# Performance work log

Hardware: AMD Instinct MI355X
Metric: run time of the kernel (lower is better)

## Reference

```python
import jax, jax.numpy as jnp
import numpy as np

GROUPS = 32
EPS = 1e-5


def group_norm(x, gamma, beta):
    # x: [b, h, w, c] NHWC; normalize over (h, w, c/GROUPS) within each group
    b, h, w, c = x.shape
    xg = x.reshape(b, h, w, GROUPS, c // GROUPS)
    mean = jnp.mean(xg, axis=(1, 2, 4), keepdims=True)
    var = jnp.var(xg, axis=(1, 2, 4), keepdims=True)
    xg = (xg - mean) * jax.lax.rsqrt(var + EPS)
    return xg.reshape(b, h, w, c) * gamma + beta


def setup_inputs() -> dict:
    key = jax.random.key(0)
    ks = jax.random.split(key, 6)
    c = 512
    s = 1.0 / np.sqrt(c)  # fan-in scaled init for conv weights
    return {
        "x": jax.random.normal(ks[0], (2, 64, 64, c), dtype=jnp.float32),
        "gamma": jnp.ones((c,), jnp.float32),
        "beta": jnp.zeros((c,), jnp.float32),
        "wq": jax.random.normal(ks[1], (c, c), jnp.float32) * s,
        "bq": jnp.zeros((c,), jnp.float32),
        "wk": jax.random.normal(ks[2], (c, c), jnp.float32) * s,
        "bk": jnp.zeros((c,), jnp.float32),
        "wv": jax.random.normal(ks[3], (c, c), jnp.float32) * s,
        "bv": jnp.zeros((c,), jnp.float32),
        "wo": jax.random.normal(ks[4], (c, c), jnp.float32) * s,
        "bo": jnp.zeros((c,), jnp.float32),
    }


def reference(x, gamma, beta, wq, bq, wk, bk, wv, bv, wo, bo):
    b, h, w, c = x.shape
    n = h * w
    hn = group_norm(x, gamma, beta)
    hn = hn.reshape(b, n, c)  # flatten spatial -> tokens
    # 1x1 convs == pointwise linear
    q = hn @ wq + bq  # [b, n, c]
    k = hn @ wk + bk
    v = hn @ wv + bv
    scores = jnp.einsum("bic,bjc->bij", q, k) * (c ** -0.5)  # [b, n, n]
    attn = jax.nn.softmax(scores, axis=-1)
    out = jnp.einsum("bij,bjc->bic", attn, v)  # [b, n, c]
    out = out @ wo + bo
    return x + out.reshape(b, h, w, c)
```

## Files before the change

### kernel.cpp

```cpp
#include <hip/hip_runtime.h>
#include <hip/hip_fp8.h>
#include <stdint.h>


typedef unsigned short u16;
typedef unsigned char u8;
typedef short s16x8 __attribute__((ext_vector_type(8)));
typedef float f32x4 __attribute__((ext_vector_type(4)));
typedef int i32x8 __attribute__((ext_vector_type(8)));
typedef float f32x16 __attribute__((ext_vector_type(16)));

#define NTOK 4096
#define CH   512

__device__ inline u16 f2bf(float f) {
  union { float f; uint32_t u; } v; v.f = f;
  uint32_t r = v.u + 0x7FFFu + ((v.u >> 16) & 1u);
  return (u16)(r >> 16);
}
__device__ inline float bf2f(u16 b) {
  union { uint32_t u; float f; } v; v.u = (uint32_t)b << 16; return v.f;
}
__device__ inline f32x4 mfma16(s16x8 a, s16x8 b, f32x4 c) {
  return __builtin_amdgcn_mfma_f32_16x16x32_bf16(a, b, c, 0, 0, 0);
}
__device__ inline f32x16 mfma_mx8(i32x8 a, i32x8 b, f32x16 c) {
  return __builtin_amdgcn_mfma_scale_f32_32x32x64_f8f6f4(
      a, b, c, 0 , 0 ,
      0, 0x7F7F7F7F, 0, 0x7F7F7F7F);
}
__device__ inline uint32_t pk_fp8x4(float e0, float e1, float e2, float e3) {
#if __has_builtin(__builtin_amdgcn_cvt_pk_fp8_f32)
  int v = __builtin_amdgcn_cvt_pk_fp8_f32(e0, e1, 0, false);
  v = __builtin_amdgcn_cvt_pk_fp8_f32(e2, e3, v, true);
  return (uint32_t)v;
#else
  __hip_fp8_e4m3 a(e0), b(e1), c(e2), d(e3);
  return (uint32_t)*(u8*)&a | ((uint32_t)*(u8*)&b << 8) |
         ((uint32_t)*(u8*)&c << 16) | ((uint32_t)*(u8*)&d << 24);
#endif
}
__device__ inline u8 f2fp8(float x) {
#if __has_builtin(__builtin_amdgcn_cvt_pk_fp8_f32)
  int v = __builtin_amdgcn_cvt_pk_fp8_f32(x, x, 0, false);
  return (u8)(v & 0xFF);
#else
  __hip_fp8_e4m3 h(x); return *(u8*)&h;
#endif
}
__device__ inline void gload_lds16(const void* g, void* l) {
  __builtin_amdgcn_global_load_lds(
      (const __attribute__((address_space(1))) unsigned*)g,
      (__attribute__((address_space(3))) unsigned*)l, 16, 0, 0);
}
__device__ inline uint4 addbf8(uint4 a, uint4 b) {
  union { uint4 v; u16 h[8]; } A, B, O; A.v = a; B.v = b;
#pragma unroll
  for (int j = 0; j < 8; j++) O.h[j] = f2bf(bf2f(A.h[j]) + bf2f(B.h[j]));
  return O.v;
}

__global__ __launch_bounds__(256) void gn_stats_kernel(
    const float* __restrict__ x, float* __restrict__ part) {
  int c = blockIdx.x, b = blockIdx.y;
  int t = threadIdx.x, g = t & 31;
  const float* xb = x + (size_t)b * NTOK * CH + (size_t)c * 64 * CH + g * 16;
  float s = 0.f, q = 0.f;
  for (int p = 0; p < 8; p++) {
    const float* ptr = xb + ((size_t)p * 8 + (t >> 5)) * CH;
#pragma unroll
    for (int j = 0; j < 4; j++) {
      float4 v = *(const float4*)(ptr + j * 4);
      s += v.x + v.y + v.z + v.w;
      q += v.x * v.x + v.y * v.y + v.z * v.z + v.w * v.w;
    }
  }
  __shared__ float ls[32][8], lq[32][8];
  ls[g][t >> 5] = s; lq[g][t >> 5] = q;
  __syncthreads();
  if (t < 32) {
    float S = 0.f, Q = 0.f;
#pragma unroll
    for (int j = 0; j < 8; j++) { S += ls[t][j]; Q += lq[t][j]; }
    float2 o; o.x = S; o.y = Q;
    *(float2*)&part[(((size_t)b * 64 + c) * 32 + t) * 2] = o;
  }
}

__global__ __launch_bounds__(256) void gn_apply_kernel(
    const float* __restrict__ x, const float* __restrict__ part,
    const float* __restrict__ gamma, const float* __restrict__ beta,
    u16* __restrict__ hn) {
  int blk = blockIdx.x, b = blk >> 9, t = threadIdx.x;
  __shared__ float msh[32], rsh[32];
  if (t < 64) {
    int g = t >> 1, half = t & 1;
    float S = 0.f, Q = 0.f;
    for (int c = half * 32; c < half * 32 + 32; c++) {
      float2 p = *(const float2*)&part[(((size_t)b * 64 + c) * 32 + g) * 2];
      S += p.x; Q += p.y;
    }
    S += __shfl_xor(S, 1, 64);
    Q += __shfl_xor(Q, 1, 64);
    if (half == 0) {
      float mean = S * (1.f / 65536.f);
      float var = Q * (1.f / 65536.f) - mean * mean;
      msh[g] = mean; rsh[g] = rsqrtf(var + 1e-5f);
    }
  }
  __syncthreads();
  size_t base = (size_t)b * NTOK * CH + (size_t)(blk & 511) * 4096 + t * 16;
  int ch0 = (t * 16) & 511;
  float mean = msh[t & 31], rstd = rsh[t & 31];
  const float* xp = x + base;
  union { u16 h[16]; uint4 v[2]; } o;
#pragma unroll
  for (int j = 0; j < 4; j++) {
    float4 xv = *(const float4*)(xp + j * 4);
    float4 gv = *(const float4*)(gamma + ch0 + j * 4);
    float4 bv = *(const float4*)(beta + ch0 + j * 4);
    o.h[j * 4 + 0] = f2bf((xv.x - mean) * rstd * gv.x + bv.x);
    o.h[j * 4 + 1] = f2bf((xv.y - mean) * rstd * gv.y + bv.y);
    o.h[j * 4 + 2] = f2bf((xv.z - mean) * rstd * gv.z + bv.z);
    o.h[j * 4 + 3] = f2bf((xv.w - mean) * rstd * gv.w + bv.w);
  }
  *(uint4*)(hn + base) = o.v[0];
  *(uint4*)(hn + base + 8) = o.v[1];
}

__global__ __launch_bounds__(256) void wprep_kernel(
    const float* w0, const float* w1, const float* w2, const float* w3,
    u16* t0, u16* t1, u16* t2, u16* t3) {
  int z = blockIdx.z;
  const float* w = z == 0 ? w0 : z == 1 ? w1 : z == 2 ? w2 : w3;
  u16* wt = z == 0 ? t0 : z == 1 ? t1 : z == 2 ? t2 : t3;
  __shared__ float tile[32][33];
  int k0 = blockIdx.x * 32, n0 = blockIdx.y * 32;
  int tx = threadIdx.x & 31, ty = threadIdx.x >> 5;
  for (int r = 0; r < 4; r++)
    tile[ty * 4 + r][tx] = w[(size_t)(k0 + ty * 4 + r) * CH + n0 + tx];
  __syncthreads();
  for (int r = 0; r < 4; r++)
    wt[(size_t)(n0 + ty * 4 + r) * CH + k0 + tx] = f2bf(tile[tx][ty * 4 + r]);
}

__global__ __launch_bounds__(256, 2) void qkv_gemm_kernel(
    const u16* __restrict__ A, const u16* __restrict__ Wcat,
    const float* __restrict__ bq, const float* __restrict__ bk,
    const float* __restrict__ bvv, u8* __restrict__ qf8, u8* __restrict__ kf8,
    u8* __restrict__ vtf8) {
  __shared__ __align__(16) u8 pool[65536];
  int m0 = blockIdx.x * 128, n0 = blockIdx.y * 128;
  int t = threadIdx.x, lane = t & 63, wave = t >> 6;
  int wx = wave & 1, wy = wave >> 1;
  int lane4 = lane >> 4;
  f32x4 acc[4][4] = {};
  const u16 *Asrc[4], *Bsrc[4];
  int dsto[4];
#pragma unroll
  for (int j = 0; j < 4; j++) {
    int u = t + j * 256, row = u >> 3, ch = (u & 7) ^ (row & 7);
    Asrc[j] = A + (size_t)(m0 + row) * CH + ch * 8;
    Bsrc[j] = Wcat + (size_t)(n0 + row) * CH + ch * 8;
    dsto[j] = u * 16;
  }
#pragma unroll
  for (int j = 0; j < 4; j++) {
    gload_lds16(Asrc[j], pool + dsto[j]);
    gload_lds16(Bsrc[j], pool + 32768 + dsto[j]);
  }
  __syncthreads();
  for (int kt = 0; kt < 8; kt++) {
    int co = (kt & 1) * 16384;
    const u16* Ac = (const u16*)(pool + co);
    const u16* Bc = (const u16*)(pool + 32768 + co);
    if (kt < 7) {
      int no = ((kt & 1) ^ 1) * 16384;
#pragma unroll
      for (int j = 0; j < 4; j++) {
        Asrc[j] += 64; Bsrc[j] += 64;
        gload_lds16(Asrc[j], pool + no + dsto[j]);
        gload_lds16(Bsrc[j], pool + 32768 + no + dsto[j]);
      }
    }
    __builtin_amdgcn_s_setprio(1);
#pragma unroll
    for (int ks = 0; ks < 2; ks++) {
      int kc = ks * 4 + lane4;
      s16x8 af[4], bf[4];
#pragma unroll
      for (int i = 0; i < 4; i++) {
        int ra = wx * 64 + i * 16 + (lane & 15);
        af[i] = *(const s16x8*)&Ac[ra * 64 + ((kc ^ (ra & 7)) << 3)];
        int rb = wy * 64 + i * 16 + (lane & 15);
        bf[i] = *(const s16x8*)&Bc[rb * 64 + ((kc ^ (rb & 7)) << 3)];
      }
#pragma unroll
      for (int mi = 0; mi < 4; mi++)
#pragma unroll
        for (int ni = 0; ni < 4; ni++)
          acc[mi][ni] = mfma16(af[mi], bf[ni], acc[mi][ni]);
    }
    __builtin_amdgcn_s_setprio(0);
    __syncthreads();
  }
  int proj = n0 >> 9;
  int r0l = wx * 64 + lane4 * 4;
  if (proj <= 1) {
    u8* O = proj == 0 ? qf8 : kf8;
    const float* bias = proj == 0 ? bq : bk;
#pragma unroll
    for (int mi = 0; mi < 4; mi++)
#pragma unroll
      for (int ni = 0; ni < 4; ni++) {
        int colp = (n0 & 511) + wy * 64 + ni * 16 + (lane & 15);
        float bv = bias[colp];
#pragma unroll
        for (int r = 0; r < 4; r++)
          O[(size_t)(m0 + r0l + mi * 16 + r) * CH + colp] =
              f2fp8(acc[mi][ni][r] + bv);
      }
  } else {
#pragma unroll
    for (int mi = 0; mi < 4; mi++)
#pragma unroll
      for (int ni = 0; ni < 4; ni++) {
        int colp = (n0 & 511) + wy * 64 + ni * 16 + (lane & 15);
        float bv = bvv[colp];
        int row = m0 + r0l + mi * 16;
        int bb = row >> 12, nn = row & 4095;
        uint32_t p = pk_fp8x4(acc[mi][ni][0] + bv, acc[mi][ni][1] + bv,
                              acc[mi][ni][2] + bv, acc[mi][ni][3] + bv);
        *(uint32_t*)&vtf8[((size_t)bb * CH + colp) * NTOK + nn] = p;
      }
  }
}

__global__ __launch_bounds__(256) void gemm_out_kernel(
    const u16* __restrict__ A, const u16* __restrict__ A2,
    const u16* __restrict__ Wt, const float* __restrict__ bias,
    float* __restrict__ out, const float* __restrict__ xres) {
  __shared__ __align__(16) u16 As[128 * 40];
  __shared__ __align__(16) u16 Bs[64 * 40];
  int m0 = blockIdx.x * 128, n0 = blockIdx.y * 64;
  int t = threadIdx.x, lane = t & 63, wave = t >> 6;
  int wm = wave >> 1, wn = wave & 1;
  f32x4 acc[4][2] = {};
  int arow = t >> 2, ac = t & 3;
  size_t aoff = (size_t)(m0 + arow) * CH + ac * 8;
  const u16* Bg = Wt + (size_t)(n0 + arow) * CH + ac * 8;
  uint4 a0 = addbf8(*(const uint4*)(A + aoff), *(const uint4*)(A2 + aoff));
  uint4 a1 = addbf8(*(const uint4*)(A + aoff + 64 * CH),
                    *(const uint4*)(A2 + aoff + 64 * CH));
  uint4 b0 = *(const uint4*)Bg;
  for (int kt = 0; kt < 16; kt++) {
    __syncthreads();
    *(uint4*)&As[(size_t)arow * 40 + ac * 8] = a0;
    *(uint4*)&As[(size_t)(arow + 64) * 40 + ac * 8] = a1;
    *(uint4*)&Bs[(size_t)arow * 40 + ac * 8] = b0;
    if (kt < 15) {
      aoff += 32; Bg += 32;
      a0 = addbf8(*(const uint4*)(A + aoff), *(const uint4*)(A2 + aoff));
      a1 = addbf8(*(const uint4*)(A + aoff + 64 * CH),
                  *(const uint4*)(A2 + aoff + 64 * CH));
      b0 = *(const uint4*)Bg;
    }
    __syncthreads();
    s16x8 af[4], bfr[2];
#pragma unroll
    for (int i = 0; i < 4; i++)
      af[i] = *(const s16x8*)&As[(wm * 64 + i * 16 + (lane & 15)) * 40 + (lane >> 4) * 8];
#pragma unroll
    for (int j = 0; j < 2; j++)
      bfr[j] = *(const s16x8*)&Bs[(wn * 32 + j * 16 + (lane & 15)) * 40 + (lane >> 4) * 8];
    __builtin_amdgcn_s_setprio(1);
#pragma unroll
    for (int mi = 0; mi < 4; mi++)
#pragma unroll
      for (int ni = 0; ni < 2; ni++)
        acc[mi][ni] = mfma16(af[mi], bfr[ni], acc[mi][ni]);
    __builtin_amdgcn_s_setprio(0);
  }
  int r0l = wm * 64 + ((lane >> 4) * 4);
  int c0l = wn * 32 + (lane & 15);
#pragma unroll
  for (int mi = 0; mi < 4; mi++)
#pragma unroll
    for (int ni = 0; ni < 2; ni++) {
      int col = n0 + c0l + ni * 16;
      float bv = bias[col];
#pragma unroll
      for (int r = 0; r < 4; r++) {
        size_t idx = (size_t)(m0 + r0l + mi * 16 + r) * CH + col;
        out[idx] = xres[idx] + acc[mi][ni][r] + bv;
      }
    }
}

__global__ __launch_bounds__(256, 2) void s_gemm_kernel(
    const u8* __restrict__ qf8, const u8* __restrict__ kf8,
    u8* __restrict__ S, float* __restrict__ lpart) {
  const float QS = 0.044194173824159216f;
  __shared__ __align__(16) u8 pool[65536];
  int bz = blockIdx.z;
  const u8* qb = qf8 + (size_t)bz * NTOK * CH;
  const u8* kb = kf8 + (size_t)bz * NTOK * CH;
  u8* Sg = S + (size_t)bz * NTOK * NTOK;
  float* lp = lpart + (size_t)bz * 64 * NTOK;
  int m0 = blockIdx.x * 128, n0 = blockIdx.y * 128;
  int t = threadIdx.x, lane = t & 63, wave = t >> 6;
  int wmx = wave & 1, wy = wave >> 1;
  int lh = lane >> 5;
  f32x16 acc[2][2] = {};
  const u8 *Asrc[4], *Bsrc[4];
  int dsto[4];
#pragma unroll
  for (int j = 0; j < 4; j++) {
    int u = t + j * 256, row = u >> 3, ch = (u & 7) ^ (row & 7);
    Asrc[j] = kb + (size_t)(n0 + row) * CH + ch * 16;
    Bsrc[j] = qb + (size_t)(m0 + row) * CH + ch * 16;
    dsto[j] = u * 16;
  }
#pragma unroll
  for (int j = 0; j < 4; j++) {
    gload_lds16(Asrc[j], pool + dsto[j]);
    gload_lds16(Bsrc[j], pool + 32768 + dsto[j]);
  }
  __syncthreads();
  for (int kt = 0; kt < 4; kt++) {
    int co = (kt & 1) * 16384;
    const u8* Ac = pool + co;
    const u8* Bc = pool + 32768 + co;
    if (kt < 3) {
      int no = ((kt & 1) ^ 1) * 16384;
#pragma unroll
      for (int j = 0; j < 4; j++) {
        Asrc[j] += 128; Bsrc[j] += 128;
        gload_lds16(Asrc[j], pool + no + dsto[j]);
        gload_lds16(Bsrc[j], pool + 32768 + no + dsto[j]);
      }
    }
    __builtin_amdgcn_s_setprio(1);
#pragma unroll
    for (int kh = 0; kh < 2; kh++) {
      int cb = kh * 4 + lh * 2;
      union { i32x8 v; uint4 qq[2]; } bu[2];
#pragma unroll
      for (int bj = 0; bj < 2; bj++) {
        int rb = wmx * 64 + bj * 32 + (lane & 31);
        const u8* bp = &Bc[rb * 128];
        bu[bj].qq[0] = *(const uint4*)&bp[(cb ^ (rb & 7)) << 4];
        bu[bj].qq[1] = *(const uint4*)&bp[((cb + 1) ^ (rb & 7)) << 4];
      }
#pragma unroll
      for (int ai = 0; ai < 2; ai++) {
        int ra = wy * 64 + ai * 32 + (lane & 31);
        union { i32x8 v; uint4 qq[2]; } au;
        const u8* ap = &Ac[ra * 128];
        au.qq[0] = *(const uint4*)&ap[(cb ^ (ra & 7)) << 4];
        au.qq[1] = *(const uint4*)&ap[((cb + 1) ^ (ra & 7)) << 4];
#pragma unroll
        for (int bj = 0; bj < 2; bj++)
          acc[ai][bj] = mfma_mx8(au.v, bu[bj].v, acc[ai][bj]);
      }
    }
    __builtin_amdgcn_s_setprio(0);
    __syncthreads();
  }
  uint32_t* Stile = (uint32_t*)pool;
  float psum[2] = {};
#pragma unroll
  for (int ai = 0; ai < 2; ai++) {
#pragma unroll
    for (int bj = 0; bj < 2; bj++) {
      int ml = wmx * 64 + bj * 32 + (lane & 31);
#pragma unroll
      for (int qd = 0; qd < 4; qd++) {
        float e0 = __expf(acc[ai][bj][qd * 4 + 0] * QS);
        float e1 = __expf(acc[ai][bj][qd * 4 + 1] * QS);
        float e2 = __expf(acc[ai][bj][qd * 4 + 2] * QS);
        float e3 = __expf(acc[ai][bj][qd * 4 + 3] * QS);
        psum[bj] += e0 + e1 + e2 + e3;
        int nw = wy * 16 + ai * 8 + qd * 2 + lh;
        Stile[ml * 32 + (nw ^ ((ml & 7) << 2))] = pk_fp8x4(e0, e1, e2, e3);
      }
    }
  }
#pragma unroll
  for (int bj = 0; bj < 2; bj++) {
    float v = psum[bj];
    v += __shfl_xor(v, 32, 64);
    if (lane < 32) {
      int m = m0 + wmx * 64 + bj * 32 + lane;
      lp[(size_t)((n0 >> 6) + wy) * NTOK + m] = v;
    }
  }
  __syncthreads();
#pragma unroll
  for (int p = 0; p < 4; p++) {
    int row = (t >> 3) + p * 32;
    int g = t & 7;
    int w0 = (g * 4) ^ ((row & 7) << 2);
    uint4 v;
    v.x = Stile[row * 32 + w0 + 0];
    v.y = Stile[row * 32 + w0 + 1];
    v.z = Stile[row * 32 + w0 + 2];
    v.w = Stile[row * 32 + w0 + 3];
    *(uint4*)&Sg[(size_t)(m0 + row) * NTOK + n0 + g * 16] = v;
  }
}

__global__ __launch_bounds__(256, 2) void pv_gemm_kernel(
    const u8* __restrict__ S, const u8* __restrict__ vtf8,
    const float* __restrict__ lpart, u16* __restrict__ part0,
    u16* __restrict__ part1) {
  __shared__ __align__(16) u8 Asw[2][16384];
  __shared__ __align__(16) u8 Bsw[2][16384];
  __shared__ float linv_s[128];
  int flat = blockIdx.x + 32 * blockIdx.y + 128 * blockIdx.z;
  int xcd = flat & 7, u = flat >> 3;
  int m_t = xcd * 4 + (u & 3);
  int n_i = (u >> 2) & 3;
  int spb = u >> 4, sp = spb & 1, b = spb >> 1;
  int m0 = m_t * 128, n0 = n_i * 128, kbase = sp * 2048;
  const u8* Sb = S + (size_t)b * NTOK * NTOK;
  const u8* vb = vtf8 + (size_t)b * CH * NTOK;
  const float* lp = lpart + (size_t)b * 64 * NTOK;
  int t = threadIdx.x, lane = t & 63, wave = t >> 6;
  int wm = wave >> 1, wn = wave & 1;
  int lh = lane >> 5;
  f32x16 acc[2][2] = {};
  const u8 *Asrc[4], *Bsrc[4];
  int uoff[4];
#pragma unroll
  for (int j = 0; j < 4; j++) {
    int uu = t + j * 256, row = uu >> 3, ch = (uu & 7) ^ (row & 7);
    Asrc[j] = Sb + (size_t)(m0 + row) * NTOK + kbase + ch * 16;
    Bsrc[j] = vb + (size_t)(n0 + row) * NTOK + kbase + ch * 16;
    uoff[j] = uu * 16;
  }
#pragma unroll
  for (int j = 0; j < 4; j++) {
    gload_lds16(Asrc[j], &Asw[0][uoff[j]]);
    gload_lds16(Bsrc[j], &Bsw[0][uoff[j]]);
  }
  __syncthreads();
  int cur = 0;
  for (int kt = 0; kt < 16; kt++) {
    if (kt < 15) {
#pragma unroll
      for (int j = 0; j < 4; j++) {
        Asrc[j] += 128; Bsrc[j] += 128;
        gload_lds16(Asrc[j], &Asw[cur ^ 1][uoff[j]]);
        gload_lds16(Bsrc[j], &Bsw[cur ^ 1][uoff[j]]);
      }
    }
    __builtin_amdgcn_s_setprio(1);
#pragma unroll
    for (int kh = 0; kh < 2; kh++) {
      int cb = kh * 4 + lh * 2;
      union { i32x8 v; uint4 qq[2]; } bu[2];
#pragma unroll
      for (int ni = 0; ni < 2; ni++) {
        int rb = wn * 64 + ni * 32 + (lane & 31);
        const u8* bp = &Bsw[cur][rb * 128];
        bu[ni].qq[0] = *(const uint4*)&bp[(cb ^ (rb & 7)) << 4];
        bu[ni].qq[1] = *(const uint4*)&bp[((cb + 1) ^ (rb & 7)) << 4];
      }
#pragma unroll
      for (int mi = 0; mi < 2; mi++) {
        int ra = wm * 64 + mi * 32 + (lane & 31);
        union { i32x8 v; uint4 qq[2]; } au;
        const u8* ap = &Asw[cur][ra * 128];
        au.qq[0] = *(const uint4*)&ap[(cb ^ (ra & 7)) << 4];
        au.qq[1] = *(const uint4*)&ap[((cb + 1) ^ (ra & 7)) << 4];
#pragma unroll
        for (int ni = 0; ni < 2; ni++)
          acc[mi][ni] = mfma_mx8(au.v, bu[ni].v, acc[mi][ni]);
      }
    }
    __builtin_amdgcn_s_setprio(0);
    __syncthreads();
    cur ^= 1;
  }
  if (t < 128) {
    float s = 0.f;
#pragma unroll 8
    for (int c = 0; c < 64; c++) s += lp[(size_t)c * NTOK + m0 + t];
    linv_s[t] = 1.f / s;
  }
  __syncthreads();
  u16* Od = (sp ? part1 : part0) + (size_t)b * NTOK * CH;
#pragma unroll
  for (int mi = 0; mi < 2; mi++)
#pragma unroll
    for (int ni = 0; ni < 2; ni++)
#pragma unroll
      for (int reg = 0; reg < 16; reg++) {
        int crow = (reg & 3) + 8 * (reg >> 2) + 4 * lh;
        int gr = wm * 64 + mi * 32 + crow;
        Od[(size_t)(m0 + gr) * CH + n0 + wn * 64 + ni * 32 + (lane & 31)] =
            f2bf(acc[mi][ni][reg] * linv_s[gr]);
      }
}

extern "C" void kernel_launch(void* const* d_in, const int* in_sizes, int n_in,
                              void* d_out, int out_size, void* d_ws, size_t ws_size,
                              hipStream_t stream) {
  const float* x     = (const float*)d_in[0];
  const float* gamma = (const float*)d_in[1];
  const float* beta  = (const float*)d_in[2];
  const float* wq    = (const float*)d_in[3];
  const float* bq    = (const float*)d_in[4];
  const float* wk    = (const float*)d_in[5];
  const float* bk    = (const float*)d_in[6];
  const float* wv    = (const float*)d_in[7];
  const float* bv    = (const float*)d_in[8];
  const float* wo    = (const float*)d_in[9];
  const float* bo    = (const float*)d_in[10];

  char* ws = (char*)d_ws;
  u16* hn   = (u16*)(ws + 0);
  u16* q    = (u16*)(ws + 8388608);
  u8*  vtf8 = (u8*)(ws + 25165824);
  u16* wqt  = (u16*)(ws + 33554432);
  u16* wkt  = (u16*)(ws + 34078720);
  u16* wvt  = (u16*)(ws + 34603008);
  u16* wot  = (u16*)(ws + 35127296);
  u8*  S    = (u8*)(ws + 35651584);
  float* lpart = (float*)(ws + 71303168);
  u8*  qf8  = (u8*)(ws + 75497472);
  u8*  kf8  = (u8*)(ws + 79691776);

  float* gnpart = (float*)q;

  gn_stats_kernel<<<dim3(64, 2), 256, 0, stream>>>(x, gnpart);
  wprep_kernel<<<dim3(16, 16, 4), 256, 0, stream>>>(wq, wk, wv, wo, wqt, wkt, wvt, wot);
  gn_apply_kernel<<<1024, 256, 0, stream>>>(x, gnpart, gamma, beta, hn);
  qkv_gemm_kernel<<<dim3(64, 12), 256, 0, stream>>>(hn, wqt, bq, bk, bv, qf8, kf8, vtf8);
  s_gemm_kernel<<<dim3(32, 32, 2), 256, 0, stream>>>(qf8, kf8, S, lpart);
  pv_gemm_kernel<<<dim3(32, 4, 4), 256, 0, stream>>>(S, vtf8, lpart, hn, q);
  gemm_out_kernel<<<dim3(64, 8), 256, 0, stream>>>(hn, q, wot, bo, (float*)d_out, x);
}
```

Before: 115.2 us.

## Widen output GEMM tile, pack fp8 Q/K stores, use exp2 in softmax

The output projection GEMM tile grows from 128x64 to 128x128, so each block loads twice as much weight and does four MFMA columns per wave. That improves reuse of the A operand (hn plus the attention output) but halves the grid to 256 blocks. The Q/K epilogue now combines four fp8 bytes across lanes with shuffles and writes them as one 32-bit store instead of byte stores. The S-GEMM softmax uses exp2f with a log2(e)-scaled constant instead of __expf.

After: 117.5 us. No clear change (+2.0%).

```diff
diff --git a/kernel.cpp b/kernel.cpp
--- a/kernel.cpp
+++ b/kernel.cpp
@@ -206,6 +206,7 @@
   }
   int proj = n0 >> 9;
   int r0l = wx * 64 + lane4 * 4;
+  int lsh = (lane & 3) * 8;
   if (proj <= 1) {
     u8* O = proj == 0 ? qf8 : kf8;
     const float* bias = proj == 0 ? bq : bk;
@@ -216,9 +217,13 @@
         int colp = (n0 & 511) + wy * 64 + ni * 16 + (lane & 15);
         float bv = bias[colp];
 #pragma unroll
-        for (int r = 0; r < 4; r++)
-          O[(size_t)(m0 + r0l + mi * 16 + r) * CH + colp] =
-              f2fp8(acc[mi][ni][r] + bv);
+        for (int r = 0; r < 4; r++) {
+          uint32_t piece = (uint32_t)f2fp8(acc[mi][ni][r] + bv) << lsh;
+          piece |= __shfl_xor(piece, 1);
+          piece |= __shfl_xor(piece, 2);
+          if ((lane & 3) == 0)
+            *(uint32_t*)&O[(size_t)(m0 + r0l + mi * 16 + r) * CH + colp] = piece;
+        }
       }
   } else {
 #pragma unroll
@@ -241,52 +246,52 @@
     const u16* __restrict__ Wt, const float* __restrict__ bias,
     float* __restrict__ out, const float* __restrict__ xres) {
   __shared__ __align__(16) u16 As[128 * 40];
-  __shared__ __align__(16) u16 Bs[64 * 40];
-  int m0 = blockIdx.x * 128, n0 = blockIdx.y * 64;
+  __shared__ __align__(16) u16 Bs[128 * 40];
+  int m0 = blockIdx.x * 128, n0 = blockIdx.y * 128;
   int t = threadIdx.x, lane = t & 63, wave = t >> 6;
   int wm = wave >> 1, wn = wave & 1;
-  f32x4 acc[4][2] = {};
+  f32x4 acc[4][4] = {};
   int arow = t >> 2, ac = t & 3;
-  size_t aoff = (size_t)(m0 + arow) * CH + ac * 8;
-  const u16* Bg = Wt + (size_t)(n0 + arow) * CH + ac * 8;
-  uint4 a0 = addbf8(*(const uint4*)(A + aoff), *(const uint4*)(A2 + aoff));
-  uint4 a1 = addbf8(*(const uint4*)(A + aoff + 64 * CH),
-                    *(const uint4*)(A2 + aoff + 64 * CH));
-  uint4 b0 = *(const uint4*)Bg;
+  size_t aoff0 = (size_t)(m0 + arow) * CH + ac * 8;
+  size_t aoff1 = (size_t)(m0 + arow + 64) * CH + ac * 8;
+  const u16* Bg0 = Wt + (size_t)(n0 + arow) * CH + ac * 8;
+  const u16* Bg1 = Wt + (size_t)(n0 + arow + 64) * CH + ac * 8;
+  uint4 a0 = addbf8(*(const uint4*)(A + aoff0), *(const uint4*)(A2 + aoff0));
+  uint4 a1 = addbf8(*(const uint4*)(A + aoff1), *(const uint4*)(A2 + aoff1));
+  uint4 b0 = *(const uint4*)Bg0, b1 = *(const uint4*)Bg1;
   for (int kt = 0; kt < 16; kt++) {
     __syncthreads();
     *(uint4*)&As[(size_t)arow * 40 + ac * 8] = a0;
     *(uint4*)&As[(size_t)(arow + 64) * 40 + ac * 8] = a1;
     *(uint4*)&Bs[(size_t)arow * 40 + ac * 8] = b0;
+    *(uint4*)&Bs[(size_t)(arow + 64) * 40 + ac * 8] = b1;
     if (kt < 15) {
-      aoff += 32; Bg += 32;
-      a0 = addbf8(*(const uint4*)(A + aoff), *(const uint4*)(A2 + aoff));
-      a1 = addbf8(*(const uint4*)(A + aoff + 64 * CH),
-                  *(const uint4*)(A2 + aoff + 64 * CH));
-      b0 = *(const uint4*)Bg;
+      aoff0 += 32; aoff1 += 32; Bg0 += 32; Bg1 += 32;
+      a0 = addbf8(*(const uint4*)(A + aoff0), *(const uint4*)(A2 + aoff0));
+      a1 = addbf8(*(const uint4*)(A + aoff1), *(const uint4*)(A2 + aoff1));
+      b0 = *(const uint4*)Bg0; b1 = *(const uint4*)Bg1;
     }
     __syncthreads();
-    s16x8 af[4], bfr[2];
-#pragma unroll
-    for (int i = 0; i < 4; i++)
+    s16x8 af[4], bfr[4];
+#pragma unroll
+    for (int i = 0; i < 4; i++) {
       af[i] = *(const s16x8*)&As[(wm * 64 + i * 16 + (lane & 15)) * 40 + (lane >> 4) * 8];
-#pragma unroll
-    for (int j = 0; j < 2; j++)
-      bfr[j] = *(const s16x8*)&Bs[(wn * 32 + j * 16 + (lane & 15)) * 40 + (lane >> 4) * 8];
+      bfr[i] = *(const s16x8*)&Bs[(wn * 64 + i * 16 + (lane & 15)) * 40 + (lane >> 4) * 8];
+    }
     __builtin_amdgcn_s_setprio(1);
 #pragma unroll
     for (int mi = 0; mi < 4; mi++)
 #pragma unroll
-      for (int ni = 0; ni < 2; ni++)
+      for (int ni = 0; ni < 4; ni++)
         acc[mi][ni] = mfma16(af[mi], bfr[ni], acc[mi][ni]);
     __builtin_amdgcn_s_setprio(0);
   }
   int r0l = wm * 64 + ((lane >> 4) * 4);
-  int c0l = wn * 32 + (lane & 15);
+  int c0l = wn * 64 + (lane & 15);
 #pragma unroll
   for (int mi = 0; mi < 4; mi++)
 #pragma unroll
-    for (int ni = 0; ni < 2; ni++) {
+    for (int ni = 0; ni < 4; ni++) {
       int col = n0 + c0l + ni * 16;
       float bv = bias[col];
 #pragma unroll
@@ -300,7 +305,7 @@
 __global__ __launch_bounds__(256, 2) void s_gemm_kernel(
     const u8* __restrict__ qf8, const u8* __restrict__ kf8,
     u8* __restrict__ S, float* __restrict__ lpart) {
-  const float QS = 0.044194173824159216f;
+  const float QSL2 = 0.06376275879949354f;
   __shared__ __align__(16) u8 pool[65536];
   int bz = blockIdx.z;
   const u8* qb = qf8 + (size_t)bz * NTOK * CH;
@@ -376,10 +381,10 @@
       int ml = wmx * 64 + bj * 32 + (lane & 31);
 #pragma unroll
       for (int qd = 0; qd < 4; qd++) {
-        float e0 = __expf(acc[ai][bj][qd * 4 + 0] * QS);
-        float e1 = __expf(acc[ai][bj][qd * 4 + 1] * QS);
-        float e2 = __expf(acc[ai][bj][qd * 4 + 2] * QS);
-        float e3 = __expf(acc[ai][bj][qd * 4 + 3] * QS);
+        float e0 = exp2f(acc[ai][bj][qd * 4 + 0] * QSL2);
+        float e1 = exp2f(acc[ai][bj][qd * 4 + 1] * QSL2);
+        float e2 = exp2f(acc[ai][bj][qd * 4 + 2] * QSL2);
+        float e3 = exp2f(acc[ai][bj][qd * 4 + 3] * QSL2);
         psum[bj] += e0 + e1 + e2 + e3;
         int nw = wy * 16 + ai * 8 + qd * 2 + lh;
         Stile[ml * 32 + (nw ^ ((ml & 7) << 2))] = pk_fp8x4(e0, e1, e2, e3);
@@ -540,5 +545,5 @@
   qkv_gemm_kernel<<<dim3(64, 12), 256, 0, stream>>>(hn, wqt, bq, bk, bv, qf8, kf8, vtf8);
   s_gemm_kernel<<<dim3(32, 32, 2), 256, 0, stream>>>(qf8, kf8, S, lpart);
   pv_gemm_kernel<<<dim3(32, 4, 4), 256, 0, stream>>>(S, vtf8, lpart, hn, q);
-  gemm_out_kernel<<<dim3(64, 8), 256, 0, stream>>>(hn, q, wot, bo, (float*)d_out, x);
-}
+  gemm_out_kernel<<<dim3(64, 4), 256, 0, stream>>>(hn, q, wot, bo, (float*)d_out, x);
+}
```
